# Optimization experiments

Measured on AMD Instinct MI355X. Metric: run time of the kernel, lower is better.

Reference implementation:

```python
import jax, jax.numpy as jnp
import numpy as np

VOCAB, E, H, B, T = 400000, 300, 256, 128, 256
G = 3 * H  # gate width


def _gru_dir(x, w_ih, w_hh, b_ih, b_hh, reverse):
    """Single-direction GRU over x: [B,T,in] -> [B,T,H]. PyTorch gate order r,z,n."""
    xg = jnp.einsum('bti,gi->tbg', x, w_ih) + b_ih  # [T,B,3H] precomputed input gates
    h0 = jnp.zeros((x.shape[0], w_hh.shape[1]), x.dtype)

    def step(h, xg_t):
        hg = h @ w_hh.T + b_hh
        xr, xz, xn = jnp.split(xg_t, 3, axis=-1)
        hr, hz, hn = jnp.split(hg, 3, axis=-1)
        r = jax.nn.sigmoid(xr + hr)
        z = jax.nn.sigmoid(xz + hz)
        n = jnp.tanh(xn + r * hn)
        h_new = (1.0 - z) * n + z * h
        return h_new, h_new

    _, ys = jax.lax.scan(step, h0, xg, reverse=reverse)  # ys: [T,B,H] in original time order
    return jnp.transpose(ys, (1, 0, 2))


def _bidir_layer(x, w_ih_f, w_hh_f, b_ih_f, b_hh_f, w_ih_b, w_hh_b, b_ih_b, b_hh_b):
    f = _gru_dir(x, w_ih_f, w_hh_f, b_ih_f, b_hh_f, reverse=False)
    b = _gru_dir(x, w_ih_b, w_hh_b, b_ih_b, b_hh_b, reverse=True)
    return jnp.concatenate([f, b], axis=-1)  # [B,T,2H]


def setup_inputs() -> dict:
    key = jax.random.key(0)
    ks = jax.random.split(key, 12)
    s = 0.05
    return {
        'overview': jax.random.randint(ks[0], (B, T), 0, VOCAB),
        'emb': jax.random.normal(ks[1], (VOCAB, E), jnp.float32),
        # layer 0 (input dim E), index 0=fwd, 1=bwd
        'w_ih0': jax.random.normal(ks[2], (2, G, E), jnp.float32) * s,
        'w_hh0': jax.random.normal(ks[3], (2, G, H), jnp.float32) * s,
        'b_ih0': jnp.zeros((2, G), jnp.float32),
        'b_hh0': jnp.zeros((2, G), jnp.float32),
        # layers 1..2 (input dim 2H)
        'w_ih': jax.random.normal(ks[4], (2, 2, G, 2 * H), jnp.float32) * s,
        'w_hh': jax.random.normal(ks[5], (2, 2, G, H), jnp.float32) * s,
        'b_ih': jnp.zeros((2, 2, G), jnp.float32),
        'b_hh': jnp.zeros((2, 2, G), jnp.float32),
        'lin_w': jax.random.normal(ks[6], (18, 2 * H), jnp.float32) * s,
        'lin_b': jnp.zeros((18,), jnp.float32),
    }


def reference(overview, emb, w_ih0, w_hh0, b_ih0, b_hh0, w_ih, w_hh, b_ih, b_hh, lin_w, lin_b):
    x = emb[overview]  # [B,T,E]
    x = _bidir_layer(x, w_ih0[0], w_hh0[0], b_ih0[0], b_hh0[0],
                     w_ih0[1], w_hh0[1], b_ih0[1], b_hh0[1])
    for l in range(2):  # fixed 2 additional layers (n_layers=3); dropout off at inference
        x = _bidir_layer(x, w_ih[l, 0], w_hh[l, 0], b_ih[l, 0], b_hh[l, 0],
                         w_ih[l, 1], w_hh[l, 1], b_ih[l, 1], b_hh[l, 1])
    last = x[:, -1, :]  # [B, 2H]
    return last @ lin_w.T + lin_b  # [B, 18]
```

## Files before the change

kernel.cpp:

```cpp
#include <hip/hip_runtime.h>
#include <cstdint>
#include <cstddef>

typedef float f32x4 __attribute__((ext_vector_type(4)));
typedef short s16x8 __attribute__((ext_vector_type(8)));
typedef unsigned short u16x4 __attribute__((ext_vector_type(4)));

#define T_LEN 256
#define B_SZ  128

__device__ __forceinline__ float bf2f(unsigned short u){
  union { unsigned int i; float f; } v; v.i = ((unsigned int)u) << 16; return v.f;
}
__device__ __forceinline__ unsigned short f2bf(float f){
  union { float f; unsigned int i; } v; v.f = f;
  return (unsigned short)((v.i + 0x7FFFu + ((v.i >> 16) & 1u)) >> 16);
}
__device__ __forceinline__ float fast_sigmoid(float x){
  return __builtin_amdgcn_rcpf(1.0f + __builtin_amdgcn_exp2f(-1.44269504088896341f * x));
}
__device__ __forceinline__ float fast_tanh(float x){
  return 1.0f - 2.0f * __builtin_amdgcn_rcpf(1.0f + __builtin_amdgcn_exp2f(2.88539008177792681f * x));
}

__global__ void prep_kernel(const float* __restrict__ w_ih0, const float* __restrict__ w_hh0,
                            const float* __restrict__ b_ih0, const float* __restrict__ b_hh0,
                            const float* __restrict__ w_ih,  const float* __restrict__ w_hh,
                            const float* __restrict__ b_ih,  const float* __restrict__ b_hh,
                            unsigned short* __restrict__ wih0b, unsigned short* __restrict__ wihb,
                            unsigned short* __restrict__ whhb,  float* __restrict__ bihc){
  const int S1 = 2*768*320;
  const int S2 = 2*2*768*512;
  const int S3 = 6*768*256;
  const int S4 = 3*1536;
  int idx = blockIdx.x * 256 + threadIdx.x;
  if (idx < S1){
    int k = idx % 320, r = idx / 320;
    wih0b[idx] = (k < 300) ? f2bf(w_ih0[r*300 + k]) : (unsigned short)0;
  } else if (idx < S1 + S2){
    int i = idx - S1; wihb[i] = f2bf(w_ih[i]);
  } else if (idx < S1 + S2 + S3){
    int i = idx - S1 - S2;
    const int L0 = 2*768*256;
    whhb[i] = f2bf(i < L0 ? w_hh0[i] : w_hh[i - L0]);
  } else if (idx < S1 + S2 + S3 + S4){
    int i = idx - S1 - S2 - S3;
    int l = i / 1536, n = i % 1536, g = n % 768;
    float v = (l == 0) ? b_ih0[n] : b_ih[(l-1)*1536 + n];
    if (g < 512) v += (l == 0) ? b_hh0[n] : b_hh[(l-1)*1536 + n];
    bihc[i] = v;
  }
}

__global__ void gather_kernel(const int* __restrict__ overview, const float* __restrict__ emb,
                              unsigned short* __restrict__ x0){
  const int m = blockIdx.x;
  const int t = m >> 7, b = m & 127;
  const int row = overview[b * T_LEN + t];
  const float* src = emb + (size_t)row * 300;
  unsigned short* dst = x0 + (size_t)m * 320;
  for (int i = threadIdx.x; i < 80; i += 64){
    u16x4 o;
    if (i < 75){
      const f32x4 v = *(const f32x4*)(src + i*4);
      o[0] = f2bf(v[0]); o[1] = f2bf(v[1]); o[2] = f2bf(v[2]); o[3] = f2bf(v[3]);
    } else { o[0] = o[1] = o[2] = o[3] = 0; }
    *(u16x4*)(dst + i*4) = o;
  }
}

__global__ __launch_bounds__(256, 2) void gemm_xg(
    const unsigned short* __restrict__ A, const unsigned short* __restrict__ Bw,
    const float* __restrict__ bias, unsigned short* __restrict__ xg, const int K){
  __shared__ unsigned short a_t[128*40];
  __shared__ unsigned short b_t[128*40];
  const int tid = threadIdx.x;
  const int lane = tid & 63, wv = tid >> 6;
  const int l15 = lane & 15, quad = lane >> 4;
  const int m0 = blockIdx.x * 128, n0 = blockIdx.y * 128;
  const int mW = (wv >> 1) * 64, nW = (wv & 1) * 64;
  const int r0 = tid >> 2, c = (tid & 3) * 8;

  f32x4 acc[4][4];
#pragma unroll
  for (int i = 0; i < 4; ++i)
#pragma unroll
    for (int j = 0; j < 4; ++j) acc[i][j] = (f32x4){0.f,0.f,0.f,0.f};

  for (int kk = 0; kk < K; kk += 32){
    __syncthreads();
#pragma unroll
    for (int h = 0; h < 128; h += 64){
      *(s16x8*)&a_t[(r0+h)*40 + c] = *(const s16x8*)(A  + (size_t)(m0+r0+h)*K + kk + c);
      *(s16x8*)&b_t[(r0+h)*40 + c] = *(const s16x8*)(Bw + (size_t)(n0+r0+h)*K + kk + c);
    }
    __syncthreads();
    s16x8 af[4], bf[4];
#pragma unroll
    for (int i = 0; i < 4; ++i){
      af[i] = *(const s16x8*)&a_t[(mW + i*16 + l15)*40 + quad*8];
      bf[i] = *(const s16x8*)&b_t[(nW + i*16 + l15)*40 + quad*8];
    }
#pragma unroll
    for (int i = 0; i < 4; ++i)
#pragma unroll
      for (int j = 0; j < 4; ++j)
        acc[i][j] = __builtin_amdgcn_mfma_f32_16x16x32_bf16(af[i], bf[j], acc[i][j], 0, 0, 0);
  }

#pragma unroll
  for (int j = 0; j < 4; ++j){
    const int n = n0 + nW + j*16 + l15;
    const float bv = bias[n];
    const int dir = (n >= 768) ? 1 : 0;
    const int g = n - dir*768;
    const int gc = g >> 2, gl = g & 3;
#pragma unroll
    for (int i = 0; i < 4; ++i){
      const int mbase = m0 + mW + i*16 + quad*4;
#pragma unroll
      for (int r = 0; r < 4; ++r){
        const int m = mbase + r;
        const int t = m >> 7, b = m & 127;
        const int goff = ((gc ^ (b & 15)) << 2) | gl;
        xg[((size_t)(t*2 + dir)*128 + b) * 768 + goff] = f2bf(acc[i][j][r] + bv);
      }
    }
  }
}

__global__ __launch_bounds__(256, 1) void rec_kernel(
    const unsigned short* __restrict__ xg,
    const unsigned short* __restrict__ whh2,
    const float* __restrict__ bhh2,
    unsigned short* __restrict__ y){
  extern __shared__ unsigned short sm[];
  unsigned short* w_lds  = sm;
  unsigned short* h_lds  = sm + 4*2*16*264;
  unsigned short* xg_lds = h_lds + 2*16*264;

  const int tid  = threadIdx.x;
  const int lane = tid & 63;
  const int wv   = tid >> 6;
  const int l15  = lane & 15;
  const int quad = lane >> 4;
  const int bg   = blockIdx.x & 7;
  const int dir  = blockIdx.x >> 3;
  const int bgBase = bg * 16;

  const unsigned short* whh = whh2 + dir * (768*256);

  f32x4 bn[4];
#pragma unroll
  for (int jt = 0; jt < 4; ++jt)
    bn[jt] = *(const f32x4*)(bhh2 + dir*768 + 512 + wv*64 + jt*16 + quad*4);

  for (int i = tid; i < 16*264; i += 256) h_lds[i] = 0;

  s16x8 wreg[10][8];
#pragma unroll
  for (int i = 0; i < 10; ++i){
    const int gt = i >> 2, jt = i & 3;
    const unsigned short* src = whh + (size_t)(gt*256 + wv*64 + jt*16 + l15) * 256;
#pragma unroll
    for (int ks = 0; ks < 8; ++ks)
      wreg[i][ks] = *(const s16x8*)(src + ks*32 + quad*8);
  }
#pragma unroll
  for (int ti = 0; ti < 2; ++ti){
    const int i = 10 + ti, gt = i >> 2, jt = i & 3;
    const int row = lane >> 2;
    const int col = (lane & 3) * 64;
    const unsigned short* src = whh + (size_t)(gt*256 + wv*64 + jt*16 + row) * 256 + col;
    unsigned short* dst = w_lds + ((wv*2 + ti)*16 + row) * 264 + col;
#pragma unroll
    for (int c8 = 0; c8 < 8; ++c8)
      *(s16x8*)(dst + c8*8) = *(const s16x8*)(src + c8*8);
  }

  float hreg[16];
#pragma unroll
  for (int i = 0; i < 16; ++i) hreg[i] = 0.0f;

  auto stage = [&](int t, int buf){
    const char* g = (const char*)(xg + ((size_t)(t*2 + dir)*128 + bgBase) * 768);
    char* l = (char*)(xg_lds + buf * (16*768));
#pragma unroll
    for (int j = 0; j < 6; ++j){
      const int k = wv*6 + j;
      __builtin_amdgcn_global_load_lds(
          (const __attribute__((address_space(1))) unsigned int*)(g + k*1024 + (size_t)lane*16),
          (__attribute__((address_space(3))) unsigned int*)(l + k*1024), 16, 0, 0);
    }
  };

  stage(dir ? (T_LEN - 1) : 0, 0);
  asm volatile("s_waitcnt vmcnt(0) lgkmcnt(0)" ::: "memory");
  __builtin_amdgcn_s_barrier();
  __builtin_amdgcn_sched_barrier(0);

  for (int s = 0; s < T_LEN; ++s){
    const int cur = s & 1;
    const int t = dir ? (T_LEN - 1 - s) : s;

    if (s + 1 < T_LEN) stage(dir ? (T_LEN - 2 - s) : (s + 1), cur ^ 1);
    __builtin_amdgcn_sched_barrier(0);

    s16x8 bfr[8];
    const unsigned short* hbase = h_lds + cur*(16*264) + l15*264;
#pragma unroll
    for (int ks = 0; ks < 8; ++ks)
      bfr[ks] = *(const s16x8*)(hbase + ks*32 + quad*8);

    f32x4 acc[12];
#pragma unroll
    for (int i = 0; i < 12; ++i) acc[i] = (f32x4){0.f,0.f,0.f,0.f};
#pragma unroll
    for (int i = 0; i < 10; ++i)
#pragma unroll
      for (int ks = 0; ks < 8; ++ks)
        acc[i] = __builtin_amdgcn_mfma_f32_16x16x32_bf16(wreg[i][ks], bfr[ks], acc[i], 0, 0, 0);
#pragma unroll
    for (int ti = 0; ti < 2; ++ti)
#pragma unroll
      for (int ks = 0; ks < 8; ++ks){
        s16x8 af = *(const s16x8*)(w_lds + ((wv*2 + ti)*16 + l15)*264 + ks*32 + quad*8);
        acc[10+ti] = __builtin_amdgcn_mfma_f32_16x16x32_bf16(af, bfr[ks], acc[10+ti], 0, 0, 0);
      }

    const unsigned short* curx = xg_lds + cur*(16*768) + l15*768;
    unsigned short* hwb = h_lds + (cur^1)*(16*264) + l15*264;
#pragma unroll
    for (int jt = 0; jt < 4; ++jt){
      const int off0 = (wv*16 + ((jt*4 + quad) ^ l15)) * 4;
      u16x4 xr4 = *(const u16x4*)(curx + off0);
      u16x4 xz4 = *(const u16x4*)(curx + off0 + 256);
      u16x4 xn4 = *(const u16x4*)(curx + off0 + 512);
      f32x4 ra = acc[jt], za = acc[4+jt], na = acc[8+jt];
      u16x4 hw;
#pragma unroll
      for (int r = 0; r < 4; ++r){
        float rr = fast_sigmoid(bf2f(xr4[r]) + ra[r]);
        float zz = fast_sigmoid(bf2f(xz4[r]) + za[r]);
        float nn = fast_tanh(bf2f(xn4[r]) + rr * (na[r] + bn[jt][r]));
        float hv = nn + zz * (hreg[jt*4 + r] - nn);
        hreg[jt*4 + r] = hv;
        hw[r] = f2bf(hv);
      }
      *(u16x4*)(hwb + wv*64 + jt*16 + quad*4) = hw;
      *(u16x4*)(y + ((size_t)t*128 + bgBase + l15) * 512 + dir*256 + wv*64 + jt*16 + quad*4) = hw;
    }

    asm volatile("s_waitcnt vmcnt(4) lgkmcnt(0)" ::: "memory");
    __builtin_amdgcn_s_barrier();
    __builtin_amdgcn_sched_barrier(0);
  }
}

__global__ void final_kernel(const unsigned short* __restrict__ y, const float* __restrict__ lin_w,
                             const float* __restrict__ lin_b, float* __restrict__ out){
  const int b = blockIdx.x, lane = threadIdx.x;
  s16x8 hv = *(const s16x8*)(y + ((size_t)((T_LEN-1)*128 + b)) * 512 + lane*8);
  float hf[8];
#pragma unroll
  for (int i = 0; i < 8; ++i) hf[i] = bf2f((unsigned short)hv[i]);
  float p[18];
#pragma unroll
  for (int o = 0; o < 18; ++o) p[o] = 0.0f;
#pragma unroll
  for (int i = 0; i < 8; ++i)
#pragma unroll
    for (int o = 0; o < 18; ++o) p[o] += hf[i] * lin_w[o*512 + lane*8 + i];
#pragma unroll
  for (int o = 0; o < 18; ++o){
    float v = p[o];
    for (int off = 32; off > 0; off >>= 1) v += __shfl_xor(v, off, 64);
    if (lane == 0) out[b*18 + o] = v + lin_b[o];
  }
}

extern "C" void kernel_launch(void* const* d_in, const int* in_sizes, int n_in,
                              void* d_out, int out_size, void* d_ws, size_t ws_size,
                              hipStream_t stream){
  const int*   overview = (const int*)  d_in[0];
  const float* emb   = (const float*)d_in[1];
  const float* w_ih0 = (const float*)d_in[2];
  const float* w_hh0 = (const float*)d_in[3];
  const float* b_ih0 = (const float*)d_in[4];
  const float* b_hh0 = (const float*)d_in[5];
  const float* w_ih  = (const float*)d_in[6];
  const float* w_hh  = (const float*)d_in[7];
  const float* b_ih  = (const float*)d_in[8];
  const float* b_hh  = (const float*)d_in[9];
  const float* lin_w = (const float*)d_in[10];
  const float* lin_b = (const float*)d_in[11];
  float* out = (float*)d_out;

  char* ws = (char*)d_ws;
  size_t off = 0;
  auto alloc = [&](size_t bytes) -> char* {
    char* p = ws + off; off += (bytes + 511) & ~(size_t)511; return p;
  };
  unsigned short* x0    = (unsigned short*)alloc((size_t)32768*320*2);
  unsigned short* wih0b = (unsigned short*)alloc((size_t)2*768*320*2);
  unsigned short* wihb  = (unsigned short*)alloc((size_t)2*2*768*512*2);
  unsigned short* whhb  = (unsigned short*)alloc((size_t)6*768*256*2);
  float*          bihc  = (float*)         alloc((size_t)3*1536*4);
  unsigned short* xgb   = (unsigned short*)alloc((size_t)256*2*128*768*2);
  unsigned short* ya    = (unsigned short*)alloc((size_t)32768*512*2);
  unsigned short* yb    = (unsigned short*)alloc((size_t)32768*512*2);

  const size_t REC_LDS = (size_t)(4*2*16*264 + 2*16*264 + 2*16*768) * 2;
  hipFuncSetAttribute((const void*)rec_kernel,
                      hipFuncAttributeMaxDynamicSharedMemorySize, (int)REC_LDS);

  prep_kernel<<<dim3(12690), 256, 0, stream>>>(w_ih0, w_hh0, b_ih0, b_hh0,
                                               w_ih, w_hh, b_ih, b_hh,
                                               wih0b, wihb, whhb, bihc);
  gather_kernel<<<dim3(32768), 64, 0, stream>>>(overview, emb, x0);

  gemm_xg<<<dim3(256, 12), 256, 0, stream>>>(x0, wih0b, bihc, xgb, 320);
  rec_kernel<<<dim3(16), 256, REC_LDS, stream>>>(xgb, whhb, b_hh0, ya);
  gemm_xg<<<dim3(256, 12), 256, 0, stream>>>(ya, wihb, bihc + 1536, xgb, 512);
  rec_kernel<<<dim3(16), 256, REC_LDS, stream>>>(xgb, whhb + 2*768*256, b_hh, yb);
  gemm_xg<<<dim3(256, 12), 256, 0, stream>>>(yb, wihb + (size_t)2*768*512, bihc + 2*1536, xgb, 512);
  rec_kernel<<<dim3(16), 256, REC_LDS, stream>>>(xgb, whhb + 4*768*256, b_hh + 1536, ya);

  final_kernel<<<dim3(128), 64, 0, stream>>>(ya, lin_w, lin_b, out);
}
```

Measured before the change: 2.879 ms.

## Triple-buffer input-gate prefetch and interleave h loads with MFMA in GRU recurrence

The recurrent kernel now keeps three LDS buffers for the precomputed input gates and prefetches two timesteps ahead instead of one. The wait count is relaxed so global loads have more time to land. The MFMA loop is reordered to load one h fragment per k-slice and issue all twelve gate tiles against it, which cuts live registers. Address arithmetic for the xg source and y output becomes pointer increments. The cost is more LDS per block and more complex vmcnt bookkeeping, which risks ordering mistakes with the interleaved y stores.

```diff
diff --git a/kernel.cpp b/kernel.cpp
--- a/kernel.cpp
+++ b/kernel.cpp
@@ -182,8 +182,8 @@
 #pragma unroll
   for (int i = 0; i < 16; ++i) hreg[i] = 0.0f;
 
-  auto stage = [&](int t, int buf){
-    const char* g = (const char*)(xg + ((size_t)(t*2 + dir)*128 + bgBase) * 768);
+  auto stage = [&](const unsigned short* src_base, int buf){
+    const char* g = (const char*)src_base;
     char* l = (char*)(xg_lds + buf * (16*768));
 #pragma unroll
     for (int j = 0; j < 6; ++j){
@@ -194,42 +194,50 @@
     }
   };
 
-  stage(dir ? (T_LEN - 1) : 0, 0);
-  asm volatile("s_waitcnt vmcnt(0) lgkmcnt(0)" ::: "memory");
+  const int t0 = dir ? (T_LEN - 1) : 0;
+  const ptrdiff_t step_x = dir ? -(ptrdiff_t)(2*128*768) : (ptrdiff_t)(2*128*768);
+  const ptrdiff_t step_y = dir ? -(ptrdiff_t)(128*512)   : (ptrdiff_t)(128*512);
+  const unsigned short* xg0 = xg + ((size_t)(t0*2 + dir)*128 + bgBase) * 768;
+  unsigned short* yptr = y + ((size_t)t0*128 + bgBase + l15) * 512 + dir*256 + wv*64 + quad*4;
+
+  stage(xg0, 0);
+  stage(xg0 + step_x, 1);
+  const unsigned short* sptr = xg0 + 2*step_x;
+
+  asm volatile("s_waitcnt vmcnt(6) lgkmcnt(0)" ::: "memory");
   __builtin_amdgcn_s_barrier();
   __builtin_amdgcn_sched_barrier(0);
 
+  int c3 = 0;
+  int b3 = 2;
   for (int s = 0; s < T_LEN; ++s){
-    const int cur = s & 1;
-    const int t = dir ? (T_LEN - 1 - s) : s;
-
-    if (s + 1 < T_LEN) stage(dir ? (T_LEN - 2 - s) : (s + 1), cur ^ 1);
+    const int cur2 = s & 1;
+
+    if (s + 2 < T_LEN){
+      stage(sptr, b3);
+      sptr += step_x;
+    }
     __builtin_amdgcn_sched_barrier(0);
 
-    s16x8 bfr[8];
-    const unsigned short* hbase = h_lds + cur*(16*264) + l15*264;
-#pragma unroll
-    for (int ks = 0; ks < 8; ++ks)
-      bfr[ks] = *(const s16x8*)(hbase + ks*32 + quad*8);
-
+    const unsigned short* hbase = h_lds + cur2*(16*264) + l15*264;
     f32x4 acc[12];
 #pragma unroll
     for (int i = 0; i < 12; ++i) acc[i] = (f32x4){0.f,0.f,0.f,0.f};
 #pragma unroll
-    for (int i = 0; i < 10; ++i)
-#pragma unroll
-      for (int ks = 0; ks < 8; ++ks)
-        acc[i] = __builtin_amdgcn_mfma_f32_16x16x32_bf16(wreg[i][ks], bfr[ks], acc[i], 0, 0, 0);
-#pragma unroll
-    for (int ti = 0; ti < 2; ++ti)
-#pragma unroll
-      for (int ks = 0; ks < 8; ++ks){
+    for (int ks = 0; ks < 8; ++ks){
+      const s16x8 bfr = *(const s16x8*)(hbase + ks*32 + quad*8);
+#pragma unroll
+      for (int i = 0; i < 10; ++i)
+        acc[i] = __builtin_amdgcn_mfma_f32_16x16x32_bf16(wreg[i][ks], bfr, acc[i], 0, 0, 0);
+#pragma unroll
+      for (int ti = 0; ti < 2; ++ti){
         s16x8 af = *(const s16x8*)(w_lds + ((wv*2 + ti)*16 + l15)*264 + ks*32 + quad*8);
-        acc[10+ti] = __builtin_amdgcn_mfma_f32_16x16x32_bf16(af, bfr[ks], acc[10+ti], 0, 0, 0);
+        acc[10+ti] = __builtin_amdgcn_mfma_f32_16x16x32_bf16(af, bfr, acc[10+ti], 0, 0, 0);
       }
-
-    const unsigned short* curx = xg_lds + cur*(16*768) + l15*768;
-    unsigned short* hwb = h_lds + (cur^1)*(16*264) + l15*264;
+    }
+
+    const unsigned short* curx = xg_lds + c3*(16*768) + l15*768;
+    unsigned short* hwb = h_lds + (cur2^1)*(16*264) + l15*264;
 #pragma unroll
     for (int jt = 0; jt < 4; ++jt){
       const int off0 = (wv*16 + ((jt*4 + quad) ^ l15)) * 4;
@@ -248,10 +256,14 @@
         hw[r] = f2bf(hv);
       }
       *(u16x4*)(hwb + wv*64 + jt*16 + quad*4) = hw;
-      *(u16x4*)(y + ((size_t)t*128 + bgBase + l15) * 512 + dir*256 + wv*64 + jt*16 + quad*4) = hw;
-    }
-
-    asm volatile("s_waitcnt vmcnt(4) lgkmcnt(0)" ::: "memory");
+      *(u16x4*)(yptr + jt*16) = hw;
+    }
+    yptr += step_y;
+    c3 = (c3 == 2) ? 0 : (c3 + 1);
+    b3 = (b3 == 2) ? 0 : (b3 + 1);
+
+    if (s + 2 < T_LEN) asm volatile("s_waitcnt vmcnt(10) lgkmcnt(0)" ::: "memory");
+    else               asm volatile("s_waitcnt vmcnt(4) lgkmcnt(0)"  ::: "memory");
     __builtin_amdgcn_s_barrier();
     __builtin_amdgcn_sched_barrier(0);
   }
@@ -310,7 +322,7 @@
   unsigned short* ya    = (unsigned short*)alloc((size_t)32768*512*2);
   unsigned short* yb    = (unsigned short*)alloc((size_t)32768*512*2);
 
-  const size_t REC_LDS = (size_t)(4*2*16*264 + 2*16*264 + 2*16*768) * 2;
+  const size_t REC_LDS = (size_t)(4*2*16*264 + 2*16*264 + 3*16*768) * 2;
   hipFuncSetAttribute((const void*)rec_kernel,
                       hipFuncAttributeMaxDynamicSharedMemorySize, (int)REC_LDS);
 
```

Result: faster. 2.807 ms (-2.5%).
